# Kernel tuning notes

Hardware: AMD Instinct MI355X
Metric: run time of the kernel (lower is better)

The kernel has to match this reference:

```python
import jax, jax.numpy as jnp
import numpy as np

N_NODES = 50000
N_EDGES = 800000
IN_CH = 256
OUT_CH = 128
HID = 2 * OUT_CH  # 256
N_GRAPHS = 64


def setup_inputs() -> dict:
    key = jax.random.key(0)
    k = jax.random.split(key, 8)
    x = jax.random.normal(k[0], (N_NODES, IN_CH), dtype=jnp.float32)
    edge_index = jax.random.randint(k[1], (2, N_EDGES), 0, N_NODES, dtype=jnp.int64)
    batch = jnp.sort(jax.random.randint(k[2], (N_NODES,), 0, N_GRAPHS, dtype=jnp.int64))
    # GCNConv parameters (glorot-ish init)
    W1 = jax.random.normal(k[3], (IN_CH, HID), dtype=jnp.float32) / np.sqrt(IN_CH)
    b1 = jnp.zeros((HID,), dtype=jnp.float32)
    W2 = jax.random.normal(k[4], (HID, OUT_CH), dtype=jnp.float32) / np.sqrt(HID)
    b2 = jnp.zeros((OUT_CH,), dtype=jnp.float32)
    return {"x": x, "W1": W1, "b1": b1, "W2": W2, "b2": b2,
            "edge_index": edge_index, "batch": batch}


def _gcn_conv(x, W, b, src, dst, n):
    """PyG GCNConv: transform, then sym-normalized aggregation with self-loops."""
    h = x @ W  # [N, F_out]
    # degree over destination nodes, including the added self-loop
    deg = jnp.zeros((n,), dtype=h.dtype).at[dst].add(1.0) + 1.0
    dinv = jax.lax.rsqrt(deg)
    norm = dinv[src] * dinv[dst]            # [E]
    agg = jnp.zeros_like(h).at[dst].add(h[src] * norm[:, None])
    agg = agg + h * (1.0 / deg)[:, None]    # self-loop contribution: deg_i^{-1}
    return agg + b


def reference(x, W1, b1, W2, b2, edge_index, batch):
    src, dst = edge_index[0], edge_index[1]
    # dropout is identity in eval mode (training=False)
    h = jax.nn.elu(_gcn_conv(x, W1, b1, src, dst, N_NODES))
    h = _gcn_conv(h, W2, b2, src, dst, N_NODES)
    # global mean pool over graphs
    ones = jnp.ones((N_NODES,), dtype=h.dtype)
    counts = jax.ops.segment_sum(ones, batch, num_segments=N_GRAPHS)
    sums = jax.ops.segment_sum(h, batch, num_segments=N_GRAPHS)
    return sums / jnp.maximum(counts, 1.0)[:, None]
```

## Files before the change

### kernel.cpp

```cpp
#include <hip/hip_runtime.h>
#include <hip/hip_bf16.h>

#define N_NODES 50000
#define N_EDGES 800000
#define IN_CH 256
#define HID 256
#define OUT_CH 128
#define N_GRAPHS 64
#define SCAN_BLOCKS 196
#define M_PAD 50048
#define COUNT_BLOCKS 3125
#define CVTX_BLOCKS  12512
#define SZERO_BLOCKS 3128
#define GEMM1_BLOCKS 782
#define SELF_BLOCKS  196
#define SROW 50048
#define T2_BLOCKS 391
#define T2_KC 128
#define RED_BLOCKS 128

typedef __bf16 bf16x8 __attribute__((ext_vector_type(8)));
typedef float f32x4 __attribute__((ext_vector_type(4)));
typedef unsigned short u16x8 __attribute__((ext_vector_type(8)));

__device__ __forceinline__ float bf2f(unsigned short u) {
    union { unsigned int i; float f; } x; x.i = ((unsigned int)u) << 16; return x.f;
}
__device__ __forceinline__ unsigned short f2bf(float f) {
    union { float f; unsigned int i; } x; x.f = f;
    unsigned int r = x.i + 0x7FFFu + ((x.i >> 16) & 1u);
    return (unsigned short)(r >> 16);
}

__device__ __forceinline__ void load16(const void* g, void* l) {
    __builtin_amdgcn_global_load_lds(
        (const __attribute__((address_space(1))) void*)g,
        (__attribute__((address_space(3))) void*)l, 16, 0, 0);
}

__device__ __forceinline__ int rp(const int* __restrict__ rl,
                                  const int* __restrict__ boff, int i) {
    return rl[i] + boff[i >> 8];
}

__global__ __launch_bounds__(256) void count_cvtx_kernel(const int* __restrict__ ei,
                                                         int* __restrict__ cnt,
                                                         const float* __restrict__ x,
                                                         unsigned short* __restrict__ xb,
                                                         float* __restrict__ Sp) {
    int b = blockIdx.x;
    if (b < COUNT_BLOCKS) {
        int e = b * 256 + threadIdx.x;
        atomicAdd(&cnt[ei[N_EDGES + e]], 1);
        return;
    }
    b -= COUNT_BLOCKS;
    if (b < CVTX_BLOCKS) {
        int i = b * 256 + threadIdx.x;
        ushort4 o;
        if (i < N_NODES * (IN_CH / 4)) {
            float4 v = ((const float4*)x)[i];
            o.x = f2bf(v.x); o.y = f2bf(v.y); o.z = f2bf(v.z); o.w = f2bf(v.w);
        } else {
            o = make_ushort4(0, 0, 0, 0);
        }
        ((ushort4*)xb)[i] = o;
        return;
    }
    int i = (b - CVTX_BLOCKS) * 256 + threadIdx.x;
    ((f32x4*)Sp)[i] = (f32x4){0.f, 0.f, 0.f, 0.f};
}

__global__ __launch_bounds__(256) void scan_a_kernel(const int* __restrict__ cnt,
                                                     int* __restrict__ rl,
                                                     int* __restrict__ blocksum,
                                                     float* __restrict__ dinv,
                                                     float* __restrict__ invdeg,
                                                     int* __restrict__ fillp,
                                                     const int* __restrict__ batch,
                                                     int* __restrict__ cgr) {
    __shared__ int tmp[256];
    __shared__ int hist[64];
    int t = threadIdx.x;
    int i = blockIdx.x * 256 + t;
    if (t < 64) hist[t] = 0;
    int v = (i < N_NODES) ? cnt[i] : 0;
    int x = v;
    tmp[t] = x;
    __syncthreads();
    if (i < N_NODES) atomicAdd(&hist[batch[i] & 63], 1);
#pragma unroll
    for (int off = 1; off < 256; off <<= 1) {
        int y = (t >= off) ? tmp[t - off] : 0;
        __syncthreads();
        x += y;
        tmp[t] = x;
        __syncthreads();
    }
    if (i <= N_NODES) rl[i] = x - v;
    if (i < N_NODES) {
        float d = (float)v + 1.0f;
        dinv[i] = rsqrtf(d);
        invdeg[i] = 1.0f / d;
        fillp[i] = 0;
    }
    if (t == 255) blocksum[blockIdx.x] = x;
    if (t < 64 && hist[t]) atomicAdd(&cgr[t], hist[t]);
}

__global__ __launch_bounds__(256) void scanb_cvtw_kernel(
        const int* __restrict__ blocksum, int* __restrict__ blockoff,
        const float* __restrict__ W1, const float* __restrict__ W2,
        unsigned short* __restrict__ w1t, unsigned short* __restrict__ w2t,
        const int* __restrict__ cgr, float* __restrict__ invc) {
    int t = threadIdx.x;
    if (blockIdx.x < 384) {
        int i = blockIdx.x * 256 + t;
        if (i < HID * IN_CH) {
            int n = i >> 8, k = i & 255;
            w1t[i] = f2bf(W1[k * HID + n]);
        } else {
            int j = i - HID * IN_CH;
            int n = j >> 8, k = j & 255;
            w2t[j] = f2bf(W2[k * OUT_CH + n]);
        }
        return;
    }
    if (t < N_GRAPHS) invc[t] = 1.0f / fmaxf((float)cgr[t], 1.0f);
    __shared__ int tmp[256];
    int v = (t < SCAN_BLOCKS) ? blocksum[t] : 0;
    int x = v;
    tmp[t] = x;
    __syncthreads();
#pragma unroll
    for (int off = 1; off < 256; off <<= 1) {
        int y = (t >= off) ? tmp[t - off] : 0;
        __syncthreads();
        x += y;
        tmp[t] = x;
        __syncthreads();
    }
    if (t < SCAN_BLOCKS) blockoff[t] = x - v;
}

template <int TR>
__device__ __forceinline__ void gemm_body(const unsigned short* __restrict__ A,
                                          const unsigned short* __restrict__ Bt,
                                          unsigned short* __restrict__ C,
                                          int N, int bxx, int byy, char* As, char* Bs) {
    const int K = 256;
    int tid = threadIdx.x;
    int bm = bxx * 128;
    int bn = byy * 128;
    int lane = tid & 63, wave = tid >> 6;
    int lane15 = lane & 15, quad = lane >> 4;
    int wm0 = (wave >> 1) << 6;
    int wn0 = (wave & 1) << 6;

    int s1 = tid, s2 = tid + 256;
    int r1 = s1 >> 2, q1 = (s1 & 3) ^ ((r1 >> 1) & 3);
    int r2 = s2 >> 2, q2 = (s2 & 3) ^ ((r2 >> 1) & 3);
    const char* gA1 = (const char*)(A + (size_t)(bm + r1) * K) + (q1 << 4);
    const char* gA2 = (const char*)(A + (size_t)(bm + r2) * K) + (q2 << 4);
    const char* gB1 = (const char*)(Bt + (size_t)(bn + r1) * K) + (q1 << 4);
    const char* gB2 = (const char*)(Bt + (size_t)(bn + r2) * K) + (q2 << 4);
    char* lA1 = As + (wave << 10);
    char* lA2 = As + 4096 + (wave << 10);
    char* lB1 = Bs + (wave << 10);
    char* lB2 = Bs + 4096 + (wave << 10);

    int swm = (lane15 >> 1) & 3;
    f32x4 acc[4][4];
#pragma unroll
    for (int mt = 0; mt < 4; mt++)
#pragma unroll
        for (int nt = 0; nt < 4; nt++)
            acc[mt][nt] = (f32x4){0.f, 0.f, 0.f, 0.f};

    for (int k0 = 0; k0 < K; k0 += 32) {
        __syncthreads();
        load16(gA1 + (k0 << 1), lA1);
        load16(gA2 + (k0 << 1), lA2);
        load16(gB1 + (k0 << 1), lB1);
        load16(gB2 + (k0 << 1), lB2);
        __syncthreads();
        bf16x8 af[4], bfr[4];
#pragma unroll
        for (int t = 0; t < 4; t++) {
            int ra = wm0 + t * 16 + lane15;
            af[t] = *(const bf16x8*)(As + ra * 64 + ((quad ^ swm) << 4));
            int rb = wn0 + t * 16 + lane15;
            bfr[t] = *(const bf16x8*)(Bs + rb * 64 + ((quad ^ swm) << 4));
        }
#pragma unroll
        for (int mt = 0; mt < 4; mt++)
#pragma unroll
            for (int nt = 0; nt < 4; nt++)
                acc[mt][nt] = __builtin_amdgcn_mfma_f32_16x16x32_bf16(
                    af[mt], bfr[nt], acc[mt][nt], 0, 0, 0);
    }

#pragma unroll
    for (int mt = 0; mt < 4; mt++) {
        int rowb = bm + wm0 + mt * 16 + quad * 4;
#pragma unroll
        for (int nt = 0; nt < 4; nt++) {
            int col = bn + wn0 + nt * 16 + lane15;
            f32x4 a = acc[mt][nt];
            if (TR == 0) {
                C[(size_t)(rowb + 0) * N + col] = f2bf(a[0]);
                C[(size_t)(rowb + 1) * N + col] = f2bf(a[1]);
                C[(size_t)(rowb + 2) * N + col] = f2bf(a[2]);
                C[(size_t)(rowb + 3) * N + col] = f2bf(a[3]);
            } else {
                ushort4 o;
                o.x = f2bf(a[0]); o.y = f2bf(a[1]);
                o.z = f2bf(a[2]); o.w = f2bf(a[3]);
                *(ushort4*)(C + (size_t)col * M_PAD + rowb) = o;
            }
        }
    }
}

__global__ __launch_bounds__(256) void fill_gemm1_kernel(
        const int* __restrict__ ei,
        const int* __restrict__ rl,
        const int* __restrict__ boff,
        int* __restrict__ fillp,
        int2* __restrict__ edge2,
        const float* __restrict__ dinv,
        const float* __restrict__ invdeg,
        const int* __restrict__ batch,
        const float* __restrict__ invc,
        float* __restrict__ Sp,
        const unsigned short* __restrict__ xb,
        const unsigned short* __restrict__ w1t,
        unsigned short* __restrict__ h1b) {
    __shared__ char As[8192];
    __shared__ char Bs[8192];
    int b = blockIdx.x;
    if (b < GEMM1_BLOCKS) {
        gemm_body<0>(xb, w1t, h1b, HID, b % 391, b / 391, As, Bs);
        return;
    }
    b -= GEMM1_BLOCKS;
    if (b < COUNT_BLOCKS) {
        int e = b * 256 + threadIdx.x;
        int s = ei[e];
        int d = ei[N_EDGES + e];
        int p = rp(rl, boff, d) + atomicAdd(&fillp[d], 1);
        float w = dinv[s] * dinv[d];
        edge2[p] = make_int2(s, __float_as_int(w));
        int gd = batch[d];
        atomicAdd(&Sp[(size_t)gd * SROW + s], w * invc[gd]);
        return;
    }
    int i = (b - COUNT_BLOCKS) * 256 + threadIdx.x;
    if (i < N_NODES) {
        int g = batch[i];
        atomicAdd(&Sp[(size_t)g * SROW + i], invdeg[i] * invc[g]);
    }
}

__global__ __launch_bounds__(256) void gemm_mfma_kernel(
        const unsigned short* __restrict__ A,
        const unsigned short* __restrict__ Bt,
        unsigned short* __restrict__ C,
        int N) {
    __shared__ char As[8192];
    __shared__ char Bs[8192];
    gemm_body<1>(A, Bt, C, N, blockIdx.x, blockIdx.y, As, Bs);
}

#define ACC4(V, W) \
    acc.x += bf2f(V.x) * W; acc.y += bf2f(V.y) * W; \
    acc.z += bf2f(V.z) * W; acc.w += bf2f(V.w) * W;

__global__ __launch_bounds__(256) void agg1_kernel(const unsigned short* __restrict__ h,
                                                   const float* __restrict__ bias,
                                                   const int* __restrict__ rl,
                                                   const int* __restrict__ boff,
                                                   const int2* __restrict__ edge2,
                                                   const float* __restrict__ invdeg,
                                                   unsigned short* __restrict__ out) {
    int node = blockIdx.x * 4 + (threadIdx.x >> 6);
    int lane = threadIdx.x & 63;
    if (node >= N_NODES) {
        if (node < M_PAD)
            ((ushort4*)out)[(size_t)node * 64 + lane] = make_ushort4(0, 0, 0, 0);
        return;
    }
    const ushort4* h4 = (const ushort4*)h;
    float id = invdeg[node];
    ushort4 sv = h4[(size_t)node * 64 + lane];
    float4 acc = make_float4(bf2f(sv.x) * id, bf2f(sv.y) * id,
                             bf2f(sv.z) * id, bf2f(sv.w) * id);
    int e0 = rp(rl, boff, node);
    int e1 = rp(rl, boff, node + 1);
    int e = e0;
    for (; e + 7 < e1; e += 8) {
        int2 ed[8];
        ushort4 v[8];
#pragma unroll
        for (int j = 0; j < 8; j++) ed[j] = edge2[e + j];
#pragma unroll
        for (int j = 0; j < 8; j++) v[j] = h4[(size_t)ed[j].x * 64 + lane];
#pragma unroll
        for (int j = 0; j < 8; j++) {
            float w = __int_as_float(ed[j].y);
            ACC4(v[j], w);
        }
    }
    for (; e + 3 < e1; e += 4) {
        int2 ed[4];
        ushort4 v[4];
#pragma unroll
        for (int j = 0; j < 4; j++) ed[j] = edge2[e + j];
#pragma unroll
        for (int j = 0; j < 4; j++) v[j] = h4[(size_t)ed[j].x * 64 + lane];
#pragma unroll
        for (int j = 0; j < 4; j++) {
            float w = __int_as_float(ed[j].y);
            ACC4(v[j], w);
        }
    }
    for (; e < e1; e++) {
        int2 ed0 = edge2[e];
        float w0 = __int_as_float(ed0.y);
        ushort4 v0 = h4[(size_t)ed0.x * 64 + lane];
        ACC4(v0, w0);
    }
    float4 bb = ((const float4*)bias)[lane];
    acc.x += bb.x; acc.y += bb.y; acc.z += bb.z; acc.w += bb.w;
    acc.x = acc.x > 0.f ? acc.x : expm1f(acc.x);
    acc.y = acc.y > 0.f ? acc.y : expm1f(acc.y);
    acc.z = acc.z > 0.f ? acc.z : expm1f(acc.z);
    acc.w = acc.w > 0.f ? acc.w : expm1f(acc.w);
    ushort4 o;
    o.x = f2bf(acc.x); o.y = f2bf(acc.y); o.z = f2bf(acc.z); o.w = f2bf(acc.w);
    ((ushort4*)out)[(size_t)node * 64 + lane] = o;
}

__global__ __launch_bounds__(256) void t2_kernel(const float* __restrict__ Sp,
                                                 const unsigned short* __restrict__ h2t,
                                                 float* __restrict__ part) {
    int b = blockIdx.x;
    int k0 = b * T2_KC;
    int tid = threadIdx.x;
    int lane = tid & 63, wave = tid >> 6;
    int lane15 = lane & 15, quad = lane >> 4;
    int cb = wave << 5;
    f32x4 acc[4][2];
#pragma unroll
    for (int m = 0; m < 4; m++) {
        acc[m][0] = (f32x4){0.f, 0.f, 0.f, 0.f};
        acc[m][1] = (f32x4){0.f, 0.f, 0.f, 0.f};
    }
    const unsigned short* hr0 = h2t + (size_t)(cb + lane15) * M_PAD;
    const unsigned short* hr1 = h2t + (size_t)(cb + 16 + lane15) * M_PAD;
#pragma unroll
    for (int ks = 0; ks < T2_KC / 32; ks++) {
        int k = k0 + ks * 32 + quad * 8;
        bf16x8 b0 = *(const bf16x8*)(hr0 + k);
        bf16x8 b1 = *(const bf16x8*)(hr1 + k);
#pragma unroll
        for (int m = 0; m < 4; m++) {
            const float* ap = Sp + (size_t)(m * 16 + lane15) * SROW + k;
            f32x4 v0 = *(const f32x4*)ap;
            f32x4 v1 = *(const f32x4*)(ap + 4);
            u16x8 hu, lu;
#pragma unroll
            for (int j = 0; j < 4; j++) {
                unsigned int e0 = __float_as_uint(v0[j]);
                hu[j] = (unsigned short)(e0 >> 16);
                lu[j] = f2bf(v0[j] - __uint_as_float(e0 & 0xFFFF0000u));
                unsigned int e1 = __float_as_uint(v1[j]);
                hu[j + 4] = (unsigned short)(e1 >> 16);
                lu[j + 4] = f2bf(v1[j] - __uint_as_float(e1 & 0xFFFF0000u));
            }
            bf16x8 ah = __builtin_bit_cast(bf16x8, hu);
            bf16x8 al = __builtin_bit_cast(bf16x8, lu);
            acc[m][0] = __builtin_amdgcn_mfma_f32_16x16x32_bf16(ah, b0, acc[m][0], 0, 0, 0);
            acc[m][0] = __builtin_amdgcn_mfma_f32_16x16x32_bf16(al, b0, acc[m][0], 0, 0, 0);
            acc[m][1] = __builtin_amdgcn_mfma_f32_16x16x32_bf16(ah, b1, acc[m][1], 0, 0, 0);
            acc[m][1] = __builtin_amdgcn_mfma_f32_16x16x32_bf16(al, b1, acc[m][1], 0, 0, 0);
        }
    }
    float* pb = part + (size_t)b * (N_GRAPHS * OUT_CH);
#pragma unroll
    for (int m = 0; m < 4; m++) {
        int g0 = m * 16 + quad * 4;
#pragma unroll
        for (int nt = 0; nt < 2; nt++) {
            int c = cb + nt * 16 + lane15;
            f32x4 a = acc[m][nt];
#pragma unroll
            for (int j = 0; j < 4; j++)
                pb[(g0 + j) * OUT_CH + c] = a[j];
        }
    }
}

__global__ __launch_bounds__(256) void t2red_kernel(const float* __restrict__ part,
                                                    const float* __restrict__ b2,
                                                    const int* __restrict__ cgr,
                                                    float* __restrict__ out) {
    __shared__ float red[4][64];
    int tid = threadIdx.x;
    int q = tid >> 6, l = tid & 63;
    int o = blockIdx.x * 64 + l;
    float s = 0.f;
    for (int i = q; i < T2_BLOCKS; i += 4)
        s += part[(size_t)i * (N_GRAPHS * OUT_CH) + o];
    red[q][l] = s;
    __syncthreads();
    if (tid < 64) {
        float tot = red[0][l] + red[1][l] + red[2][l] + red[3][l];
        int g = o >> 7, c = o & 127;
        out[o] = (cgr[g] > 0) ? tot + b2[c] : 0.f;
    }
}

extern "C" void kernel_launch(void* const* d_in, const int* in_sizes, int n_in,
                              void* d_out, int out_size, void* d_ws, size_t ws_size,
                              hipStream_t stream) {
    const float* x  = (const float*)d_in[0];
    const float* W1 = (const float*)d_in[1];
    const float* b1 = (const float*)d_in[2];
    const float* W2 = (const float*)d_in[3];
    const float* b2 = (const float*)d_in[4];
    const int*   ei = (const int*)d_in[5];
    const int*   batch = (const int*)d_in[6];
    float* out = (float*)d_out;

    unsigned short* xb  = (unsigned short*)d_ws;
    unsigned short* h1b = xb  + (size_t)M_PAD * IN_CH;
    unsigned short* hBb = h1b + (size_t)M_PAD * HID;
    unsigned short* h2t = hBb + (size_t)M_PAD * HID;
    unsigned short* w1t = h2t + (size_t)OUT_CH * M_PAD;
    unsigned short* w2t = w1t + HID * IN_CH;
    float* dinv   = (float*)(w2t + OUT_CH * HID);
    float* invdeg = dinv + N_NODES;
    int*   rl     = (int*)(invdeg + N_NODES);
    int2*  edge2  = (int2*)(rl + 50016);
    int*   cnt    = (int*)(edge2 + N_EDGES);
    int*   cgr    = cnt + N_NODES;
    int*   fillp  = cgr + N_GRAPHS;
    float* Sp     = (float*)(fillp + N_NODES);
    int*   blocksum = (int*)(Sp + (size_t)N_GRAPHS * SROW);
    int*   blockoff = blocksum + 256;
    float* invc   = (float*)(blockoff + 256);
    float* part   = (float*)h1b;

    hipMemsetAsync(cnt, 0, (size_t)(N_NODES + N_GRAPHS) * 4, stream);

    count_cvtx_kernel<<<COUNT_BLOCKS + CVTX_BLOCKS + SZERO_BLOCKS, 256, 0, stream>>>(
        ei, cnt, x, xb, Sp);
    scan_a_kernel<<<SCAN_BLOCKS, 256, 0, stream>>>(cnt, rl, blocksum, dinv, invdeg,
                                                   fillp, batch, cgr);
    scanb_cvtw_kernel<<<385, 256, 0, stream>>>(blocksum, blockoff, W1, W2, w1t, w2t,
                                               cgr, invc);
    fill_gemm1_kernel<<<GEMM1_BLOCKS + COUNT_BLOCKS + SELF_BLOCKS, 256, 0, stream>>>(
        ei, rl, blockoff, fillp, edge2, dinv, invdeg, batch, invc, Sp, xb, w1t, h1b);
    agg1_kernel<<<M_PAD / 4, 256, 0, stream>>>(h1b, b1, rl, blockoff,
                                               edge2, invdeg, hBb);
    dim3 g2(M_PAD / 128, OUT_CH / 128);
    gemm_mfma_kernel<<<g2, 256, 0, stream>>>(hBb, w2t, h2t, OUT_CH);
    t2_kernel<<<T2_BLOCKS, 256, 0, stream>>>(Sp, h2t, part);
    t2red_kernel<<<RED_BLOCKS, 256, 0, stream>>>(part, b2, cgr, out);
}
```

Before: 339.1 us.

## Build pooling matrix per graph in LDS and record edge ranks during counting

The degree-count pass now stores each edge's atomic rank, so the CSR fill no longer needs a second atomic counter. The pooled-projection matrix S is built per graph and quarter in shared memory from the CSR edges and written densely, fused into the second GEMM launch. This replaces the zeroing pass and the global float atomics into S. Graph boundaries now come from the sorted batch vector instead of a histogram. The aggregation loop gains a 16-edge unroll and cheaper bf16 unpacking. The approach relies on batch being sorted and adds an erank buffer, and each graph block scans all in-edges once per quarter.

```diff
diff --git a/kernel.cpp b/kernel.cpp
--- a/kernel.cpp
+++ b/kernel.cpp
@@ -11,16 +11,18 @@
 #define M_PAD 50048
 #define COUNT_BLOCKS 3125
 #define CVTX_BLOCKS  12512
-#define SZERO_BLOCKS 3128
 #define GEMM1_BLOCKS 782
-#define SELF_BLOCKS  196
 #define SROW 50048
+#define S_QUARTER 12512
+#define GEMM2_BLOCKS 391
+#define SBUILD_BLOCKS 256
 #define T2_BLOCKS 391
 #define T2_KC 128
 #define RED_BLOCKS 128
 
 typedef __bf16 bf16x8 __attribute__((ext_vector_type(8)));
 typedef float f32x4 __attribute__((ext_vector_type(4)));
+typedef float f32x2 __attribute__((ext_vector_type(2)));
 typedef unsigned short u16x8 __attribute__((ext_vector_type(8)));
 
 __device__ __forceinline__ float bf2f(unsigned short u) {
@@ -32,6 +34,13 @@
     return (unsigned short)(r >> 16);
 }
 
+__device__ __forceinline__ float lo_f(unsigned int u) {
+    return __uint_as_float(u << 16);
+}
+__device__ __forceinline__ float hi_f(unsigned int u) {
+    return __uint_as_float(u & 0xFFFF0000u);
+}
+
 __device__ __forceinline__ void load16(const void* g, void* l) {
     __builtin_amdgcn_global_load_lds(
         (const __attribute__((address_space(1))) void*)g,
@@ -45,30 +54,24 @@
 
 __global__ __launch_bounds__(256) void count_cvtx_kernel(const int* __restrict__ ei,
                                                          int* __restrict__ cnt,
+                                                         int* __restrict__ erank,
                                                          const float* __restrict__ x,
-                                                         unsigned short* __restrict__ xb,
-                                                         float* __restrict__ Sp) {
+                                                         unsigned short* __restrict__ xb) {
     int b = blockIdx.x;
     if (b < COUNT_BLOCKS) {
         int e = b * 256 + threadIdx.x;
-        atomicAdd(&cnt[ei[N_EDGES + e]], 1);
+        erank[e] = atomicAdd(&cnt[ei[N_EDGES + e]], 1);
         return;
     }
-    b -= COUNT_BLOCKS;
-    if (b < CVTX_BLOCKS) {
-        int i = b * 256 + threadIdx.x;
-        ushort4 o;
-        if (i < N_NODES * (IN_CH / 4)) {
-            float4 v = ((const float4*)x)[i];
-            o.x = f2bf(v.x); o.y = f2bf(v.y); o.z = f2bf(v.z); o.w = f2bf(v.w);
-        } else {
-            o = make_ushort4(0, 0, 0, 0);
-        }
-        ((ushort4*)xb)[i] = o;
-        return;
-    }
-    int i = (b - CVTX_BLOCKS) * 256 + threadIdx.x;
-    ((f32x4*)Sp)[i] = (f32x4){0.f, 0.f, 0.f, 0.f};
+    int i = (b - COUNT_BLOCKS) * 256 + threadIdx.x;
+    ushort4 o;
+    if (i < N_NODES * (IN_CH / 4)) {
+        float4 v = ((const float4*)x)[i];
+        o.x = f2bf(v.x); o.y = f2bf(v.y); o.z = f2bf(v.z); o.w = f2bf(v.w);
+    } else {
+        o = make_ushort4(0, 0, 0, 0);
+    }
+    ((ushort4*)xb)[i] = o;
 }
 
 __global__ __launch_bounds__(256) void scan_a_kernel(const int* __restrict__ cnt,
@@ -76,19 +79,22 @@
                                                      int* __restrict__ blocksum,
                                                      float* __restrict__ dinv,
                                                      float* __restrict__ invdeg,
-                                                     int* __restrict__ fillp,
                                                      const int* __restrict__ batch,
-                                                     int* __restrict__ cgr) {
+                                                     int* __restrict__ rstart) {
     __shared__ int tmp[256];
-    __shared__ int hist[64];
     int t = threadIdx.x;
     int i = blockIdx.x * 256 + t;
-    if (t < 64) hist[t] = 0;
     int v = (i < N_NODES) ? cnt[i] : 0;
     int x = v;
     tmp[t] = x;
     __syncthreads();
-    if (i < N_NODES) atomicAdd(&hist[batch[i] & 63], 1);
+    if (i < N_NODES) {
+        int bg = batch[i];
+        int bp = (i > 0) ? batch[i - 1] : -1;
+        for (int g = bp + 1; g <= bg; g++) rstart[g] = i;
+        if (i == N_NODES - 1)
+            for (int g = bg + 1; g <= N_GRAPHS; g++) rstart[g] = N_NODES;
+    }
 #pragma unroll
     for (int off = 1; off < 256; off <<= 1) {
         int y = (t >= off) ? tmp[t - off] : 0;
@@ -102,17 +108,14 @@
         float d = (float)v + 1.0f;
         dinv[i] = rsqrtf(d);
         invdeg[i] = 1.0f / d;
-        fillp[i] = 0;
     }
     if (t == 255) blocksum[blockIdx.x] = x;
-    if (t < 64 && hist[t]) atomicAdd(&cgr[t], hist[t]);
 }
 
 __global__ __launch_bounds__(256) void scanb_cvtw_kernel(
         const int* __restrict__ blocksum, int* __restrict__ blockoff,
         const float* __restrict__ W1, const float* __restrict__ W2,
-        unsigned short* __restrict__ w1t, unsigned short* __restrict__ w2t,
-        const int* __restrict__ cgr, float* __restrict__ invc) {
+        unsigned short* __restrict__ w1t, unsigned short* __restrict__ w2t) {
     int t = threadIdx.x;
     if (blockIdx.x < 384) {
         int i = blockIdx.x * 256 + t;
@@ -126,7 +129,6 @@
         }
         return;
     }
-    if (t < N_GRAPHS) invc[t] = 1.0f / fmaxf((float)cgr[t], 1.0f);
     __shared__ int tmp[256];
     int v = (t < SCAN_BLOCKS) ? blocksum[t] : 0;
     int x = v;
@@ -226,13 +228,9 @@
         const int* __restrict__ ei,
         const int* __restrict__ rl,
         const int* __restrict__ boff,
-        int* __restrict__ fillp,
+        const int* __restrict__ erank,
         int2* __restrict__ edge2,
         const float* __restrict__ dinv,
-        const float* __restrict__ invdeg,
-        const int* __restrict__ batch,
-        const float* __restrict__ invc,
-        float* __restrict__ Sp,
         const unsigned short* __restrict__ xb,
         const unsigned short* __restrict__ w1t,
         unsigned short* __restrict__ h1b) {
@@ -243,38 +241,14 @@
         gemm_body<0>(xb, w1t, h1b, HID, b % 391, b / 391, As, Bs);
         return;
     }
-    b -= GEMM1_BLOCKS;
-    if (b < COUNT_BLOCKS) {
-        int e = b * 256 + threadIdx.x;
-        int s = ei[e];
-        int d = ei[N_EDGES + e];
-        int p = rp(rl, boff, d) + atomicAdd(&fillp[d], 1);
-        float w = dinv[s] * dinv[d];
-        edge2[p] = make_int2(s, __float_as_int(w));
-        int gd = batch[d];
-        atomicAdd(&Sp[(size_t)gd * SROW + s], w * invc[gd]);
-        return;
-    }
-    int i = (b - COUNT_BLOCKS) * 256 + threadIdx.x;
-    if (i < N_NODES) {
-        int g = batch[i];
-        atomicAdd(&Sp[(size_t)g * SROW + i], invdeg[i] * invc[g]);
-    }
-}
-
-__global__ __launch_bounds__(256) void gemm_mfma_kernel(
-        const unsigned short* __restrict__ A,
-        const unsigned short* __restrict__ Bt,
-        unsigned short* __restrict__ C,
-        int N) {
-    __shared__ char As[8192];
-    __shared__ char Bs[8192];
-    gemm_body<1>(A, Bt, C, N, blockIdx.x, blockIdx.y, As, Bs);
-}
-
-#define ACC4(V, W) \
-    acc.x += bf2f(V.x) * W; acc.y += bf2f(V.y) * W; \
-    acc.z += bf2f(V.z) * W; acc.w += bf2f(V.w) * W;
+    int e = (b - GEMM1_BLOCKS) * 256 + threadIdx.x;
+    if (e >= N_EDGES) return;
+    int s = ei[e];
+    int d = ei[N_EDGES + e];
+    int p = rp(rl, boff, d) + erank[e];
+    float w = dinv[s] * dinv[d];
+    edge2[p] = make_int2(s, __float_as_int(w));
+}
 
 __global__ __launch_bounds__(256) void agg1_kernel(const unsigned short* __restrict__ h,
                                                    const float* __restrict__ bias,
@@ -290,17 +264,32 @@
             ((ushort4*)out)[(size_t)node * 64 + lane] = make_ushort4(0, 0, 0, 0);
         return;
     }
-    const ushort4* h4 = (const ushort4*)h;
+    const uint2* h4 = (const uint2*)h;
     float id = invdeg[node];
-    ushort4 sv = h4[(size_t)node * 64 + lane];
-    float4 acc = make_float4(bf2f(sv.x) * id, bf2f(sv.y) * id,
-                             bf2f(sv.z) * id, bf2f(sv.w) * id);
+    uint2 sv = h4[(size_t)node * 64 + lane];
+    f32x4 acc = (f32x4){lo_f(sv.x) * id, hi_f(sv.x) * id,
+                        lo_f(sv.y) * id, hi_f(sv.y) * id};
     int e0 = rp(rl, boff, node);
     int e1 = rp(rl, boff, node + 1);
     int e = e0;
+    for (; e + 15 < e1; e += 16) {
+        int2 ed[16];
+        uint2 v[16];
+#pragma unroll
+        for (int j = 0; j < 16; j++) ed[j] = edge2[e + j];
+#pragma unroll
+        for (int j = 0; j < 16; j++) v[j] = h4[(size_t)ed[j].x * 64 + lane];
+#pragma unroll
+        for (int j = 0; j < 16; j++) {
+            float w = __int_as_float(ed[j].y);
+            f32x4 vf = (f32x4){lo_f(v[j].x), hi_f(v[j].x),
+                               lo_f(v[j].y), hi_f(v[j].y)};
+            acc += vf * w;
+        }
+    }
     for (; e + 7 < e1; e += 8) {
         int2 ed[8];
-        ushort4 v[8];
+        uint2 v[8];
 #pragma unroll
         for (int j = 0; j < 8; j++) ed[j] = edge2[e + j];
 #pragma unroll
@@ -308,12 +297,14 @@
 #pragma unroll
         for (int j = 0; j < 8; j++) {
             float w = __int_as_float(ed[j].y);
-            ACC4(v[j], w);
+            f32x4 vf = (f32x4){lo_f(v[j].x), hi_f(v[j].x),
+                               lo_f(v[j].y), hi_f(v[j].y)};
+            acc += vf * w;
         }
     }
     for (; e + 3 < e1; e += 4) {
         int2 ed[4];
-        ushort4 v[4];
+        uint2 v[4];
 #pragma unroll
         for (int j = 0; j < 4; j++) ed[j] = edge2[e + j];
 #pragma unroll
@@ -321,24 +312,69 @@
 #pragma unroll
         for (int j = 0; j < 4; j++) {
             float w = __int_as_float(ed[j].y);
-            ACC4(v[j], w);
+            f32x4 vf = (f32x4){lo_f(v[j].x), hi_f(v[j].x),
+                               lo_f(v[j].y), hi_f(v[j].y)};
+            acc += vf * w;
         }
     }
     for (; e < e1; e++) {
         int2 ed0 = edge2[e];
         float w0 = __int_as_float(ed0.y);
-        ushort4 v0 = h4[(size_t)ed0.x * 64 + lane];
-        ACC4(v0, w0);
+        uint2 v0 = h4[(size_t)ed0.x * 64 + lane];
+        f32x4 vf = (f32x4){lo_f(v0.x), hi_f(v0.x), lo_f(v0.y), hi_f(v0.y)};
+        acc += vf * w0;
     }
     float4 bb = ((const float4*)bias)[lane];
-    acc.x += bb.x; acc.y += bb.y; acc.z += bb.z; acc.w += bb.w;
-    acc.x = acc.x > 0.f ? acc.x : expm1f(acc.x);
-    acc.y = acc.y > 0.f ? acc.y : expm1f(acc.y);
-    acc.z = acc.z > 0.f ? acc.z : expm1f(acc.z);
-    acc.w = acc.w > 0.f ? acc.w : expm1f(acc.w);
+    acc[0] += bb.x; acc[1] += bb.y; acc[2] += bb.z; acc[3] += bb.w;
+    acc[0] = acc[0] > 0.f ? acc[0] : expm1f(acc[0]);
+    acc[1] = acc[1] > 0.f ? acc[1] : expm1f(acc[1]);
+    acc[2] = acc[2] > 0.f ? acc[2] : expm1f(acc[2]);
+    acc[3] = acc[3] > 0.f ? acc[3] : expm1f(acc[3]);
     ushort4 o;
-    o.x = f2bf(acc.x); o.y = f2bf(acc.y); o.z = f2bf(acc.z); o.w = f2bf(acc.w);
+    o.x = f2bf(acc[0]); o.y = f2bf(acc[1]); o.z = f2bf(acc[2]); o.w = f2bf(acc[3]);
     ((ushort4*)out)[(size_t)node * 64 + lane] = o;
+}
+
+__global__ __launch_bounds__(256) void gemm2_sbuild_kernel(
+        const unsigned short* __restrict__ A,
+        const unsigned short* __restrict__ Bt,
+        unsigned short* __restrict__ C,
+        const int2* __restrict__ edge2,
+        const int* __restrict__ rl,
+        const int* __restrict__ boff,
+        const int* __restrict__ rstart,
+        const float* __restrict__ invdeg,
+        float* __restrict__ Sp) {
+    __shared__ float srow[S_QUARTER];
+    int b = blockIdx.x;
+    if (b < GEMM2_BLOCKS) {
+        gemm_body<1>(A, Bt, C, OUT_CH, b, 0, (char*)srow, (char*)srow + 8192);
+        return;
+    }
+    int sb = b - GEMM2_BLOCKS;
+    int g = sb >> 2;
+    int base = (sb & 3) * S_QUARTER;
+    int t = threadIdx.x;
+    for (int i = t; i < S_QUARTER; i += 256) srow[i] = 0.f;
+    int n0 = rstart[g], n1 = rstart[g + 1];
+    __syncthreads();
+    int e0 = rp(rl, boff, n0);
+    int e1 = rp(rl, boff, n1);
+    for (int e = e0 + t; e < e1; e += 256) {
+        int2 ed = edge2[e];
+        unsigned int s = (unsigned int)(ed.x - base);
+        if (s < S_QUARTER)
+            atomicAdd(&srow[s], __int_as_float(ed.y));
+    }
+    __syncthreads();
+    float ic = 1.0f / fmaxf((float)(n1 - n0), 1.0f);
+    float* Sg = Sp + (size_t)g * SROW + base;
+    for (int i = t; i < S_QUARTER; i += 256) {
+        float v = srow[i];
+        int col = base + i;
+        if (col >= n0 && col < n1) v += invdeg[col];
+        Sg[i] = v * ic;
+    }
 }
 
 __global__ __launch_bounds__(256) void t2_kernel(const float* __restrict__ Sp,
@@ -403,7 +439,7 @@
 
 __global__ __launch_bounds__(256) void t2red_kernel(const float* __restrict__ part,
                                                     const float* __restrict__ b2,
-                                                    const int* __restrict__ cgr,
+                                                    const int* __restrict__ rstart,
                                                     float* __restrict__ out) {
     __shared__ float red[4][64];
     int tid = threadIdx.x;
@@ -417,7 +453,7 @@
     if (tid < 64) {
         float tot = red[0][l] + red[1][l] + red[2][l] + red[3][l];
         int g = o >> 7, c = o & 127;
-        out[o] = (cgr[g] > 0) ? tot + b2[c] : 0.f;
+        out[o] = (rstart[g + 1] > rstart[g]) ? tot + b2[c] : 0.f;
     }
 }
 
@@ -444,28 +480,25 @@
     int*   rl     = (int*)(invdeg + N_NODES);
     int2*  edge2  = (int2*)(rl + 50016);
     int*   cnt    = (int*)(edge2 + N_EDGES);
-    int*   cgr    = cnt + N_NODES;
-    int*   fillp  = cgr + N_GRAPHS;
-    float* Sp     = (float*)(fillp + N_NODES);
-    int*   blocksum = (int*)(Sp + (size_t)N_GRAPHS * SROW);
+    int*   erank  = cnt + N_NODES;
+    int*   blocksum = erank + N_EDGES;
     int*   blockoff = blocksum + 256;
-    float* invc   = (float*)(blockoff + 256);
-    float* part   = (float*)h1b;
-
-    hipMemsetAsync(cnt, 0, (size_t)(N_NODES + N_GRAPHS) * 4, stream);
-
-    count_cvtx_kernel<<<COUNT_BLOCKS + CVTX_BLOCKS + SZERO_BLOCKS, 256, 0, stream>>>(
-        ei, cnt, x, xb, Sp);
+    int*   rstart   = blockoff + 256;
+    float* Sp     = (float*)(rstart + 80);
+    float* part   = (float*)xb;
+
+    hipMemsetAsync(cnt, 0, (size_t)N_NODES * 4, stream);
+
+    count_cvtx_kernel<<<COUNT_BLOCKS + CVTX_BLOCKS, 256, 0, stream>>>(ei, cnt, erank, x, xb);
     scan_a_kernel<<<SCAN_BLOCKS, 256, 0, stream>>>(cnt, rl, blocksum, dinv, invdeg,
-                                                   fillp, batch, cgr);
-    scanb_cvtw_kernel<<<385, 256, 0, stream>>>(blocksum, blockoff, W1, W2, w1t, w2t,
-                                               cgr, invc);
-    fill_gemm1_kernel<<<GEMM1_BLOCKS + COUNT_BLOCKS + SELF_BLOCKS, 256, 0, stream>>>(
-        ei, rl, blockoff, fillp, edge2, dinv, invdeg, batch, invc, Sp, xb, w1t, h1b);
+                                                   batch, rstart);
+    scanb_cvtw_kernel<<<385, 256, 0, stream>>>(blocksum, blockoff, W1, W2, w1t, w2t);
+    fill_gemm1_kernel<<<GEMM1_BLOCKS + COUNT_BLOCKS, 256, 0, stream>>>(
+        ei, rl, blockoff, erank, edge2, dinv, xb, w1t, h1b);
     agg1_kernel<<<M_PAD / 4, 256, 0, stream>>>(h1b, b1, rl, blockoff,
                                                edge2, invdeg, hBb);
-    dim3 g2(M_PAD / 128, OUT_CH / 128);
-    gemm_mfma_kernel<<<g2, 256, 0, stream>>>(hBb, w2t, h2t, OUT_CH);
+    gemm2_sbuild_kernel<<<GEMM2_BLOCKS + SBUILD_BLOCKS, 256, 0, stream>>>(
+        hBb, w2t, h2t, edge2, rl, blockoff, rstart, invdeg, Sp);
     t2_kernel<<<T2_BLOCKS, 256, 0, stream>>>(Sp, h2t, part);
-    t2red_kernel<<<RED_BLOCKS, 256, 0, stream>>>(part, b2, cgr, out);
-}
+    t2red_kernel<<<RED_BLOCKS, 256, 0, stream>>>(part, b2, rstart, out);
+}
```

Result: faster. 297.3 us (-12.3%).
